# Performance work log

Measured on AMD Instinct MI355X. Metric: run time of the kernel, lower is better.

## Reference

```python
import jax, jax.numpy as jnp
import numpy as np
import math

D_MODEL = 1024
NUM_HEADS = 16
B, S = 2, 2048


def setup_inputs() -> dict:
    key = jax.random.key(0)
    ks = jax.random.split(key, 12)
    s = 0.02
    inp = {
        "q": jax.random.normal(ks[0], (B, S, D_MODEL), jnp.float32),
        "k": jax.random.normal(ks[1], (B, S, D_MODEL), jnp.float32),
        "v": jax.random.normal(ks[2], (B, S, D_MODEL), jnp.float32),
        "W_q": jax.random.normal(ks[3], (D_MODEL, D_MODEL), jnp.float32) * s,
        "b_q": jnp.zeros((D_MODEL,), jnp.float32),
        "W_k": jax.random.normal(ks[4], (D_MODEL, D_MODEL), jnp.float32) * s,
        "b_k": jnp.zeros((D_MODEL,), jnp.float32),
        "W_v": jax.random.normal(ks[5], (D_MODEL, D_MODEL), jnp.float32) * s,
        "b_v": jnp.zeros((D_MODEL,), jnp.float32),
        "W_o": jax.random.normal(ks[6], (D_MODEL, D_MODEL), jnp.float32) * s,
        "b_o": jnp.zeros((D_MODEL,), jnp.float32),
        # broadcastable causal mask [1,1,S,S]; masked positions are 0
        "mask": jnp.tril(jnp.ones((S, S), jnp.int32))[None, None, :, :],
    }
    return inp


def reference(q, k, v, W_q, b_q, W_k, b_k, W_v, b_v, W_o, b_o, mask):
    H, d_k = NUM_HEADS, D_MODEL // NUM_HEADS
    Bq, Sq, D = q.shape
    Sk = k.shape[1]
    # Linear projections (torch Linear: x @ W.T + b), split heads -> [B,H,S,d_k]
    qh = (q @ W_q.T + b_q).reshape(Bq, Sq, H, d_k).transpose(0, 2, 1, 3)
    kh = (k @ W_k.T + b_k).reshape(Bq, Sk, H, d_k).transpose(0, 2, 1, 3)
    vh = (v @ W_v.T + b_v).reshape(Bq, Sk, H, d_k).transpose(0, 2, 1, 3)
    # scores [B,H,Sq,Sk]
    scores = jnp.einsum("bhqd,bhkd->bhqk", qh, kh) / math.sqrt(d_k)
    scores = jnp.where(mask == 0, jnp.float32(-jnp.inf), scores)
    attn = jax.nn.softmax(scores, axis=-1)
    context = jnp.einsum("bhqk,bhkd->bhqd", attn, vh)
    context = context.transpose(0, 2, 1, 3).reshape(Bq, Sq, D)
    return context @ W_o.T + b_o
```

## Files before the change

kernel.cpp:

```cpp
#include <hip/hip_runtime.h>
#include <hip/hip_bf16.h>

using f32x4  = __attribute__((ext_vector_type(4))) float;
using short8 = __attribute__((ext_vector_type(8))) short;
using us8    = __attribute__((ext_vector_type(8))) unsigned short;
using us4    = __attribute__((ext_vector_type(4))) unsigned short;
using fl4    = __attribute__((ext_vector_type(4))) float;

__device__ __forceinline__ unsigned short f2bf(float f){
    unsigned u = __builtin_bit_cast(unsigned, f);
    u += 0x7FFF + ((u >> 16) & 1);
    return (unsigned short)(u >> 16);
}

__device__ __forceinline__ void gload16(const unsigned short* g, unsigned short* l) {
    __builtin_amdgcn_global_load_lds(
        (const __attribute__((address_space(1))) unsigned int*)g,
        (__attribute__((address_space(3))) unsigned int*)l, 16, 0, 0);
}

__global__ __launch_bounds__(256)
void conv_bf16(const float* __restrict__ s0, const float* __restrict__ s1, const float* __restrict__ s2,
               const float* __restrict__ s3, const float* __restrict__ s4, const float* __restrict__ s5,
               const float* __restrict__ s6,
               unsigned short* __restrict__ d0, unsigned short* __restrict__ d1, unsigned short* __restrict__ d2,
               unsigned short* __restrict__ d3, unsigned short* __restrict__ d4, unsigned short* __restrict__ d5,
               unsigned short* __restrict__ d6,
               int nbig4, int nsml4)
{
    const int z = blockIdx.z;
    const float* s = (z==0)?s0:(z==1)?s1:(z==2)?s2:(z==3)?s3:(z==4)?s4:(z==5)?s5:s6;
    unsigned short* d = (z==0)?d0:(z==1)?d1:(z==2)?d2:(z==3)?d3:(z==4)?d4:(z==5)?d5:d6;
    const int n4 = (z < 3) ? nbig4 : nsml4;
    const int stride = gridDim.x * blockDim.x;
    for (int i = blockIdx.x * blockDim.x + threadIdx.x; i < n4; i += stride) {
        fl4 v = ((const fl4*)s)[i];
        us4 o = { f2bf(v[0]), f2bf(v[1]), f2bf(v[2]), f2bf(v[3]) };
        ((us4*)d)[i] = o;
    }
}

template<bool OBF16>
__global__ __launch_bounds__(256, 2)
void gemm_bf16(const unsigned short* __restrict__ A0, const unsigned short* __restrict__ A1,
               const unsigned short* __restrict__ A2,
               const unsigned short* __restrict__ W0, const unsigned short* __restrict__ W1,
               const unsigned short* __restrict__ W2,
               const float* __restrict__ B0, const float* __restrict__ B1, const float* __restrict__ B2,
               void* __restrict__ O0, void* __restrict__ O1, void* __restrict__ O2,
               int M, int N, int K)
{
    const int z = blockIdx.z;
    const unsigned short* Ap = (z==0)?A0:(z==1)?A1:A2;
    const unsigned short* Wp = (z==0)?W0:(z==1)?W1:W2;
    const float* bp = (z==0)?B0:(z==1)?B1:B2;
    void* Op = (z==0)?O0:(z==1)?O1:O2;

    const int tid = threadIdx.x, lane = tid & 63, w = tid >> 6;
    const int wr = w >> 1, wc = w & 1;
    const int l15 = lane & 15, l4 = lane >> 4;
    const int bm = blockIdx.y, bn = blockIdx.x;

    __shared__ unsigned short As[2][128 * 64];
    __shared__ unsigned short Bs[2][128 * 64];

    f32x4 acc[4][4];
    #pragma unroll
    for (int i = 0; i < 4; i++)
        #pragma unroll
        for (int j = 0; j < 4; j++) acc[i][j] = (f32x4){0.f, 0.f, 0.f, 0.f};

    const int KT = K >> 6;
    const int srow = lane >> 3;
    const int scol = (lane & 7) * 8;

    auto stage = [&](int buf, int kt) {
        #pragma unroll
        for (int i = 0; i < 4; i++) {
            const int chunk = w * 4 + i;
            const int row = chunk * 8 + srow;
            gload16(Ap + (size_t)(bm * 128 + row) * K + kt * 64 + scol, &As[buf][chunk * 512]);
            gload16(Wp + (size_t)(bn * 128 + row) * K + kt * 64 + scol, &Bs[buf][chunk * 512]);
        }
    };

    stage(0, 0);
    int cur = 0;
    for (int kt = 0; kt < KT; ++kt) {
        if (kt + 1 < KT) {
            stage(cur ^ 1, kt + 1);
            asm volatile("s_waitcnt vmcnt(8)" ::: "memory");
        } else {
            asm volatile("s_waitcnt vmcnt(0)" ::: "memory");
        }
        __builtin_amdgcn_s_barrier();

        short8 af[4][2], bfr[4][2];
        #pragma unroll
        for (int mf = 0; mf < 4; mf++)
            #pragma unroll
            for (int kf = 0; kf < 2; kf++)
                af[mf][kf] = *(const short8*)&As[cur][(wr * 64 + mf * 16 + l15) * 64 + kf * 32 + l4 * 8];
        #pragma unroll
        for (int nf = 0; nf < 4; nf++)
            #pragma unroll
            for (int kf = 0; kf < 2; kf++)
                bfr[nf][kf] = *(const short8*)&Bs[cur][(wc * 64 + nf * 16 + l15) * 64 + kf * 32 + l4 * 8];
        #pragma unroll
        for (int mf = 0; mf < 4; mf++)
            #pragma unroll
            for (int nf = 0; nf < 4; nf++)
                #pragma unroll
                for (int kf = 0; kf < 2; kf++)
                    acc[mf][nf] = __builtin_amdgcn_mfma_f32_16x16x32_bf16(af[mf][kf], bfr[nf][kf], acc[mf][nf], 0, 0, 0);

        __builtin_amdgcn_s_barrier();
        cur ^= 1;
    }

    #pragma unroll
    for (int mf = 0; mf < 4; mf++) {
        int row = bm * 128 + wr * 64 + mf * 16 + l4 * 4;
        #pragma unroll
        for (int nf = 0; nf < 4; nf++) {
            int col = bn * 128 + wc * 64 + nf * 16 + l15;
            float bv = bp[col];
            #pragma unroll
            for (int r = 0; r < 4; r++) {
                float vv = acc[mf][nf][r] + bv;
                if constexpr (OBF16)
                    ((unsigned short*)Op)[(size_t)(row + r) * N + col] = f2bf(vv);
                else
                    ((float*)Op)[(size_t)(row + r) * N + col] = vv;
            }
        }
    }
}

__global__ __launch_bounds__(256, 2)
void attn_causal(const unsigned short* __restrict__ Qp,
                 const unsigned short* __restrict__ Kp,
                 const unsigned short* __restrict__ Vp,
                 unsigned short* __restrict__ Ctx)
{
    const int S = 2048, D = 1024;
    const int bh = blockIdx.y, b = bh >> 4, h = bh & 15;
    const int pairIdx = blockIdx.x;
    const int tid = threadIdx.x, w = tid >> 6, lane = tid & 63;
    const int l15 = lane & 15, l4 = lane >> 4;

    __shared__ unsigned short Ks[64 * 64];
    __shared__ unsigned short Vt[64 * 64];
    __shared__ unsigned short Ps[4][16 * 64];

    const float sc = 0.125f * 1.44269504088896f;

    for (int phase = 0; phase < 2; ++phase) {
        const int qt = (phase == 0) ? pairIdx : 31 - pairIdx;
        const int nt = qt + 1;
        const int qbase = qt * 64 + w * 16;
        const int qrow = qbase + l15;

        short8 qf[2];
        #pragma unroll
        for (int kf = 0; kf < 2; kf++)
            qf[kf] = *(const short8*)(Qp + (size_t)(b * S + qrow) * D + h * 64 + kf * 32 + l4 * 8);

        float mrow = -3.0e38f, lrow = 0.f;
        f32x4 oacc[4];
        #pragma unroll
        for (int df = 0; df < 4; df++) oacc[df] = (f32x4){0.f, 0.f, 0.f, 0.f};

        us8 krg[2], vrg[2];
        #pragma unroll
        for (int i = 0; i < 2; i++) {
            int cc = i * 256 + tid, r = cc >> 3, d0 = (cc & 7) * 8;
            krg[i] = *(const us8*)(Kp + (size_t)(b * S + r) * D + h * 64 + d0);
            vrg[i] = *(const us8*)(Vp + (size_t)(b * S + r) * D + h * 64 + d0);
        }

        for (int t = 0; t < nt; ++t) {
            __syncthreads();
            #pragma unroll
            for (int i = 0; i < 2; i++) {
                int cc = i * 256 + tid, r = cc >> 3, e = cc & 7, d0 = e * 8;
                int koff = (r * 128 + d0 * 2) ^ ((r & 7) << 4);
                *(us8*)((char*)Ks + koff) = krg[i];
                #pragma unroll
                for (int j = 0; j < 8; j++) {
                    int voff = ((d0 + j) * 128 + r * 2) ^ (e << 4);
                    *(unsigned short*)((char*)Vt + voff) = vrg[i][j];
                }
            }
            __syncthreads();

            if (t + 1 < nt) {
                #pragma unroll
                for (int i = 0; i < 2; i++) {
                    int cc = i * 256 + tid, r = cc >> 3, d0 = (cc & 7) * 8;
                    krg[i] = *(const us8*)(Kp + (size_t)(b * S + (t + 1) * 64 + r) * D + h * 64 + d0);
                    vrg[i] = *(const us8*)(Vp + (size_t)(b * S + (t + 1) * 64 + r) * D + h * 64 + d0);
                }
            }

            f32x4 sf[4];
            #pragma unroll
            for (int nf = 0; nf < 4; nf++) sf[nf] = (f32x4){0.f, 0.f, 0.f, 0.f};
            #pragma unroll
            for (int nf = 0; nf < 4; nf++)
                #pragma unroll
                for (int kf = 0; kf < 2; kf++) {
                    int row = nf * 16 + l15;
                    int off = (row * 128 + kf * 64 + l4 * 16) ^ ((row & 7) << 4);
                    short8 kfrag = *(const short8*)((const char*)Ks + off);
                    sf[nf] = __builtin_amdgcn_mfma_f32_16x16x32_bf16(kfrag, qf[kf], sf[nf], 0, 0, 0);
                }

            float pf[16];
            const bool domask = (t == nt - 1);
            #pragma unroll
            for (int nf = 0; nf < 4; nf++)
                #pragma unroll
                for (int r = 0; r < 4; r++) {
                    float x = sf[nf][r] * sc;
                    if (domask) {
                        int kv = t * 64 + nf * 16 + l4 * 4 + r;
                        if (kv > qrow) x = -3.0e38f;
                    }
                    pf[nf * 4 + r] = x;
                }

            float t8[8];
            #pragma unroll
            for (int i = 0; i < 8; i++) t8[i] = fmaxf(pf[i], pf[i + 8]);
            float t4a = fmaxf(t8[0], t8[4]), t4b = fmaxf(t8[1], t8[5]);
            float t4c = fmaxf(t8[2], t8[6]), t4d = fmaxf(t8[3], t8[7]);
            float pm = fmaxf(fmaxf(t4a, t4b), fmaxf(t4c, t4d));
            pm = fmaxf(pm, __shfl_xor(pm, 16));
            pm = fmaxf(pm, __shfl_xor(pm, 32));
            float mn = fmaxf(mrow, pm);
            float fs = exp2f(mrow - mn);
            float ps = 0.f;
            #pragma unroll
            for (int i = 0; i < 16; i++) { float e = exp2f(pf[i] - mn); pf[i] = e; ps += e; }
            ps += __shfl_xor(ps, 16);
            ps += __shfl_xor(ps, 32);
            lrow = lrow * fs + ps;
            mrow = mn;

            float fsq[4];
            #pragma unroll
            for (int r = 0; r < 4; r++) fsq[r] = __shfl(fs, l4 * 4 + r);
            #pragma unroll
            for (int df = 0; df < 4; df++)
                #pragma unroll
                for (int r = 0; r < 4; r++) oacc[df][r] *= fsq[r];

            #pragma unroll
            for (int nf = 0; nf < 4; nf++) {
                us4 pk = { f2bf(pf[nf * 4 + 0]), f2bf(pf[nf * 4 + 1]),
                           f2bf(pf[nf * 4 + 2]), f2bf(pf[nf * 4 + 3]) };
                int off = (l15 * 128 + (nf * 16 + l4 * 4) * 2) ^ ((l15 & 7) << 4);
                *(us4*)((char*)Ps[w] + off) = pk;
            }

            #pragma unroll
            for (int kf = 0; kf < 2; kf++) {
                int offp = (l15 * 128 + kf * 64 + l4 * 16) ^ ((l15 & 7) << 4);
                short8 pa = *(const short8*)((const char*)Ps[w] + offp);
                #pragma unroll
                for (int df = 0; df < 4; df++) {
                    int d = df * 16 + l15;
                    int offv = (d * 128 + kf * 64 + l4 * 16) ^ (((d >> 3) & 7) << 4);
                    short8 vb = *(const short8*)((const char*)Vt + offv);
                    oacc[df] = __builtin_amdgcn_mfma_f32_16x16x32_bf16(pa, vb, oacc[df], 0, 0, 0);
                }
            }
        }

        float inv = 1.0f / lrow;
        float invq[4];
        #pragma unroll
        for (int r = 0; r < 4; r++) invq[r] = __shfl(inv, l4 * 4 + r);
        #pragma unroll
        for (int df = 0; df < 4; df++)
            #pragma unroll
            for (int r = 0; r < 4; r++) {
                int row = qt * 64 + w * 16 + l4 * 4 + r;
                Ctx[(size_t)(b * S + row) * D + h * 64 + df * 16 + l15] = f2bf(oacc[df][r] * invq[r]);
            }
    }
}

extern "C" void kernel_launch(void* const* d_in, const int* in_sizes, int n_in,
                              void* d_out, int out_size, void* d_ws, size_t ws_size,
                              hipStream_t stream)
{
    const float* q  = (const float*)d_in[0];
    const float* k  = (const float*)d_in[1];
    const float* v  = (const float*)d_in[2];
    const float* Wq = (const float*)d_in[3];
    const float* bq = (const float*)d_in[4];
    const float* Wk = (const float*)d_in[5];
    const float* bk = (const float*)d_in[6];
    const float* Wv = (const float*)d_in[7];
    const float* bv = (const float*)d_in[8];
    const float* Wo = (const float*)d_in[9];
    const float* bo = (const float*)d_in[10];

    const int M = 4096, N = 1024, K = 1024;
    const size_t nBS = (size_t)M * N;
    const size_t nW  = (size_t)N * K;

    unsigned short* qb  = (unsigned short*)d_ws;
    unsigned short* kb  = qb  + nBS;
    unsigned short* vb  = kb  + nBS;
    unsigned short* Wqb = vb  + nBS;
    unsigned short* Wkb = Wqb + nW;
    unsigned short* Wvb = Wkb + nW;
    unsigned short* Wob = Wvb + nW;
    unsigned short* Qp  = Wob + nW;
    unsigned short* Kp  = Qp  + nBS;
    unsigned short* Vp  = Kp  + nBS;
    unsigned short* Ct  = qb;

    dim3 gc(1024, 1, 7);
    conv_bf16<<<gc, 256, 0, stream>>>(q, k, v, Wq, Wk, Wv, Wo,
                                      qb, kb, vb, Wqb, Wkb, Wvb, Wob,
                                      (int)(nBS / 4), (int)(nW / 4));

    dim3 g1(N / 128, M / 128, 3);
    gemm_bf16<true><<<g1, 256, 0, stream>>>(qb, kb, vb, Wqb, Wkb, Wvb,
                                            bq, bk, bv, Qp, Kp, Vp, M, N, K);

    dim3 g2(16, 32);
    attn_causal<<<g2, 256, 0, stream>>>(Qp, Kp, Vp, Ct);

    dim3 g3(N / 128, M / 128, 1);
    gemm_bf16<false><<<g3, 256, 0, stream>>>(Ct, Ct, Ct, Wob, Wob, Wob,
                                             bo, bo, bo, d_out, d_out, d_out, M, N, K);
}
```

Measured before the change: 263.8 us.

## Rework causal attention around 32x32 MFMA with pre-transposed V and register-resident P

Attention now uses 32x32x16 bf16 MFMA with two waves of 32 query rows each (128 threads), instead of 16x16 tiles across four waves. V is transposed once by a separate kernel so the tile load into LDS becomes vectorized rather than a scatter of single elements. The P matrix stays in registers, packed with v_cvt_pk_bf16_f32 and rearranged with v_permlane32_swap, which removes the LDS round trip for P. The cost is an extra kernel launch plus extra V traffic, and half as many threads per block, which lowers parallelism within each block.

```diff
diff --git a/kernel.cpp b/kernel.cpp
--- a/kernel.cpp
+++ b/kernel.cpp
@@ -2,6 +2,7 @@
 #include <hip/hip_bf16.h>
 
 using f32x4  = __attribute__((ext_vector_type(4))) float;
+using f32x16 = __attribute__((ext_vector_type(16))) float;
 using short8 = __attribute__((ext_vector_type(8))) short;
 using us8    = __attribute__((ext_vector_type(8))) unsigned short;
 using us4    = __attribute__((ext_vector_type(4))) unsigned short;
@@ -11,6 +12,16 @@
     unsigned u = __builtin_bit_cast(unsigned, f);
     u += 0x7FFF + ((u >> 16) & 1);
     return (unsigned short)(u >> 16);
+}
+
+__device__ __forceinline__ unsigned cvtpk_bf16(float lo, float hi){
+    unsigned r;
+    asm volatile("v_cvt_pk_bf16_f32 %0, %1, %2" : "=v"(r) : "v"(lo), "v"(hi));
+    return r;
+}
+
+__device__ __forceinline__ void pl32swap(unsigned &a, unsigned &b){
+    asm volatile("v_permlane32_swap_b32 %0, %1" : "+v"(a), "+v"(b));
 }
 
 __device__ __forceinline__ void gload16(const unsigned short* g, unsigned short* l) {
@@ -137,157 +148,191 @@
     }
 }
 
-__global__ __launch_bounds__(256, 2)
+__global__ __launch_bounds__(256)
+void transpose_v(const unsigned short* __restrict__ Vp, unsigned short* __restrict__ VpT)
+{
+    const int bh = blockIdx.y, b = bh >> 4, h = bh & 15;
+    const int s0 = blockIdx.x * 64;
+    const int tid = threadIdx.x;
+    __shared__ unsigned short T[64 * 64];
+    #pragma unroll
+    for (int i = 0; i < 2; i++) {
+        int cc = i * 256 + tid, r = cc >> 3, c = cc & 7;
+        us8 v = *(const us8*)(Vp + (size_t)(b * 2048 + s0 + r) * 1024 + h * 64 + c * 8);
+        int off = (r * 128 + c * 16) ^ ((((r & 7) ^ ((r >> 3) & 7))) << 4);
+        *(us8*)((char*)T + off) = v;
+    }
+    __syncthreads();
+    #pragma unroll
+    for (int i = 0; i < 2; i++) {
+        int cc = i * 256 + tid, d = cc >> 3, c = cc & 7;
+        us8 o;
+        #pragma unroll
+        for (int j = 0; j < 8; j++) {
+            int s = c * 8 + j;
+            int off = (s * 128 + d * 2) ^ ((((s & 7) ^ ((s >> 3) & 7))) << 4);
+            o[j] = *(const unsigned short*)((const char*)T + off);
+        }
+        *(us8*)(VpT + ((size_t)bh * 64 + d) * 2048 + s0 + c * 8) = o;
+    }
+}
+
+__global__ __launch_bounds__(128)
 void attn_causal(const unsigned short* __restrict__ Qp,
                  const unsigned short* __restrict__ Kp,
-                 const unsigned short* __restrict__ Vp,
+                 const unsigned short* __restrict__ VpT,
                  unsigned short* __restrict__ Ctx)
 {
     const int S = 2048, D = 1024;
     const int bh = blockIdx.y, b = bh >> 4, h = bh & 15;
     const int pairIdx = blockIdx.x;
     const int tid = threadIdx.x, w = tid >> 6, lane = tid & 63;
-    const int l15 = lane & 15, l4 = lane >> 4;
+    const int l31 = lane & 31, hi = lane >> 5;
 
     __shared__ unsigned short Ks[64 * 64];
     __shared__ unsigned short Vt[64 * 64];
-    __shared__ unsigned short Ps[4][16 * 64];
 
     const float sc = 0.125f * 1.44269504088896f;
 
     for (int phase = 0; phase < 2; ++phase) {
         const int qt = (phase == 0) ? pairIdx : 31 - pairIdx;
         const int nt = qt + 1;
-        const int qbase = qt * 64 + w * 16;
-        const int qrow = qbase + l15;
-
-        short8 qf[2];
-        #pragma unroll
-        for (int kf = 0; kf < 2; kf++)
-            qf[kf] = *(const short8*)(Qp + (size_t)(b * S + qrow) * D + h * 64 + kf * 32 + l4 * 8);
+        const int qrow = qt * 64 + w * 32 + l31;
+
+        short8 qf[4];
+        #pragma unroll
+        for (int ks = 0; ks < 4; ks++)
+            qf[ks] = *(const short8*)(Qp + (size_t)(b * S + qrow) * D + h * 64 + ks * 16 + hi * 8);
 
         float mrow = -3.0e38f, lrow = 0.f;
-        f32x4 oacc[4];
-        #pragma unroll
-        for (int df = 0; df < 4; df++) oacc[df] = (f32x4){0.f, 0.f, 0.f, 0.f};
-
-        us8 krg[2], vrg[2];
-        #pragma unroll
-        for (int i = 0; i < 2; i++) {
-            int cc = i * 256 + tid, r = cc >> 3, d0 = (cc & 7) * 8;
-            krg[i] = *(const us8*)(Kp + (size_t)(b * S + r) * D + h * 64 + d0);
-            vrg[i] = *(const us8*)(Vp + (size_t)(b * S + r) * D + h * 64 + d0);
+        f32x16 oacc[2];
+        #pragma unroll
+        for (int dh = 0; dh < 2; dh++)
+            #pragma unroll
+            for (int r = 0; r < 16; r++) oacc[dh][r] = 0.f;
+
+        us8 krg[4], vtrg[4];
+        #pragma unroll
+        for (int i = 0; i < 4; i++) {
+            int cc = i * 128 + tid, r = cc >> 3, c = cc & 7;
+            krg[i]  = *(const us8*)(Kp  + (size_t)(b * S + r) * D + h * 64 + c * 8);
+            vtrg[i] = *(const us8*)(VpT + ((size_t)bh * 64 + r) * 2048 + c * 8);
         }
 
         for (int t = 0; t < nt; ++t) {
             __syncthreads();
             #pragma unroll
-            for (int i = 0; i < 2; i++) {
-                int cc = i * 256 + tid, r = cc >> 3, e = cc & 7, d0 = e * 8;
-                int koff = (r * 128 + d0 * 2) ^ ((r & 7) << 4);
-                *(us8*)((char*)Ks + koff) = krg[i];
-                #pragma unroll
-                for (int j = 0; j < 8; j++) {
-                    int voff = ((d0 + j) * 128 + r * 2) ^ (e << 4);
-                    *(unsigned short*)((char*)Vt + voff) = vrg[i][j];
-                }
+            for (int i = 0; i < 4; i++) {
+                int cc = i * 128 + tid, r = cc >> 3, c = cc & 7;
+                int off = (r * 128 + c * 16) ^ ((r & 7) << 4);
+                *(us8*)((char*)Ks + off) = krg[i];
+                *(us8*)((char*)Vt + off) = vtrg[i];
             }
             __syncthreads();
 
             if (t + 1 < nt) {
                 #pragma unroll
-                for (int i = 0; i < 2; i++) {
-                    int cc = i * 256 + tid, r = cc >> 3, d0 = (cc & 7) * 8;
-                    krg[i] = *(const us8*)(Kp + (size_t)(b * S + (t + 1) * 64 + r) * D + h * 64 + d0);
-                    vrg[i] = *(const us8*)(Vp + (size_t)(b * S + (t + 1) * 64 + r) * D + h * 64 + d0);
-                }
-            }
-
-            f32x4 sf[4];
-            #pragma unroll
-            for (int nf = 0; nf < 4; nf++) sf[nf] = (f32x4){0.f, 0.f, 0.f, 0.f};
-            #pragma unroll
-            for (int nf = 0; nf < 4; nf++)
-                #pragma unroll
-                for (int kf = 0; kf < 2; kf++) {
-                    int row = nf * 16 + l15;
-                    int off = (row * 128 + kf * 64 + l4 * 16) ^ ((row & 7) << 4);
+                for (int i = 0; i < 4; i++) {
+                    int cc = i * 128 + tid, r = cc >> 3, c = cc & 7;
+                    krg[i]  = *(const us8*)(Kp  + (size_t)(b * S + (t + 1) * 64 + r) * D + h * 64 + c * 8);
+                    vtrg[i] = *(const us8*)(VpT + ((size_t)bh * 64 + r) * 2048 + (t + 1) * 64 + c * 8);
+                }
+            }
+
+            f32x16 sacc[2];
+            #pragma unroll
+            for (int kvh = 0; kvh < 2; kvh++)
+                #pragma unroll
+                for (int r = 0; r < 16; r++) sacc[kvh][r] = 0.f;
+            #pragma unroll
+            for (int kvh = 0; kvh < 2; kvh++)
+                #pragma unroll
+                for (int ks = 0; ks < 4; ks++) {
+                    int row = kvh * 32 + l31;
+                    int off = (row * 128 + ks * 32 + hi * 16) ^ ((l31 & 7) << 4);
                     short8 kfrag = *(const short8*)((const char*)Ks + off);
-                    sf[nf] = __builtin_amdgcn_mfma_f32_16x16x32_bf16(kfrag, qf[kf], sf[nf], 0, 0, 0);
-                }
-
-            float pf[16];
+                    sacc[kvh] = __builtin_amdgcn_mfma_f32_32x32x16_bf16(kfrag, qf[ks], sacc[kvh], 0, 0, 0);
+                }
+
+            float pf[2][16];
             const bool domask = (t == nt - 1);
             #pragma unroll
-            for (int nf = 0; nf < 4; nf++)
-                #pragma unroll
-                for (int r = 0; r < 4; r++) {
-                    float x = sf[nf][r] * sc;
+            for (int kvh = 0; kvh < 2; kvh++)
+                #pragma unroll
+                for (int r = 0; r < 16; r++) {
+                    float x = sacc[kvh][r] * sc;
                     if (domask) {
-                        int kv = t * 64 + nf * 16 + l4 * 4 + r;
+                        int kv = t * 64 + kvh * 32 + (r & 3) + 8 * (r >> 2) + 4 * hi;
                         if (kv > qrow) x = -3.0e38f;
                     }
-                    pf[nf * 4 + r] = x;
-                }
-
-            float t8[8];
-            #pragma unroll
-            for (int i = 0; i < 8; i++) t8[i] = fmaxf(pf[i], pf[i + 8]);
-            float t4a = fmaxf(t8[0], t8[4]), t4b = fmaxf(t8[1], t8[5]);
-            float t4c = fmaxf(t8[2], t8[6]), t4d = fmaxf(t8[3], t8[7]);
-            float pm = fmaxf(fmaxf(t4a, t4b), fmaxf(t4c, t4d));
-            pm = fmaxf(pm, __shfl_xor(pm, 16));
+                    pf[kvh][r] = x;
+                }
+
+            float pm = -3.0e38f;
+            #pragma unroll
+            for (int kvh = 0; kvh < 2; kvh++)
+                #pragma unroll
+                for (int r = 0; r < 16; r++) pm = fmaxf(pm, pf[kvh][r]);
             pm = fmaxf(pm, __shfl_xor(pm, 32));
             float mn = fmaxf(mrow, pm);
             float fs = exp2f(mrow - mn);
             float ps = 0.f;
             #pragma unroll
-            for (int i = 0; i < 16; i++) { float e = exp2f(pf[i] - mn); pf[i] = e; ps += e; }
-            ps += __shfl_xor(ps, 16);
+            for (int kvh = 0; kvh < 2; kvh++)
+                #pragma unroll
+                for (int r = 0; r < 16; r++) {
+                    float e = exp2f(pf[kvh][r] - mn);
+                    pf[kvh][r] = e;
+                    ps += e;
+                }
             ps += __shfl_xor(ps, 32);
             lrow = lrow * fs + ps;
             mrow = mn;
-
-            float fsq[4];
-            #pragma unroll
-            for (int r = 0; r < 4; r++) fsq[r] = __shfl(fs, l4 * 4 + r);
-            #pragma unroll
-            for (int df = 0; df < 4; df++)
-                #pragma unroll
-                for (int r = 0; r < 4; r++) oacc[df][r] *= fsq[r];
-
-            #pragma unroll
-            for (int nf = 0; nf < 4; nf++) {
-                us4 pk = { f2bf(pf[nf * 4 + 0]), f2bf(pf[nf * 4 + 1]),
-                           f2bf(pf[nf * 4 + 2]), f2bf(pf[nf * 4 + 3]) };
-                int off = (l15 * 128 + (nf * 16 + l4 * 4) * 2) ^ ((l15 & 7) << 4);
-                *(us4*)((char*)Ps[w] + off) = pk;
-            }
-
-            #pragma unroll
-            for (int kf = 0; kf < 2; kf++) {
-                int offp = (l15 * 128 + kf * 64 + l4 * 16) ^ ((l15 & 7) << 4);
-                short8 pa = *(const short8*)((const char*)Ps[w] + offp);
-                #pragma unroll
-                for (int df = 0; df < 4; df++) {
-                    int d = df * 16 + l15;
-                    int offv = (d * 128 + kf * 64 + l4 * 16) ^ (((d >> 3) & 7) << 4);
-                    short8 vb = *(const short8*)((const char*)Vt + offv);
-                    oacc[df] = __builtin_amdgcn_mfma_f32_16x16x32_bf16(pa, vb, oacc[df], 0, 0, 0);
-                }
-            }
-        }
-
-        float inv = 1.0f / lrow;
-        float invq[4];
-        #pragma unroll
-        for (int r = 0; r < 4; r++) invq[r] = __shfl(inv, l4 * 4 + r);
-        #pragma unroll
-        for (int df = 0; df < 4; df++)
-            #pragma unroll
-            for (int r = 0; r < 4; r++) {
-                int row = qt * 64 + w * 16 + l4 * 4 + r;
-                Ctx[(size_t)(b * S + row) * D + h * 64 + df * 16 + l15] = f2bf(oacc[df][r] * invq[r]);
+            #pragma unroll
+            for (int dh = 0; dh < 2; dh++)
+                #pragma unroll
+                for (int r = 0; r < 16; r++) oacc[dh][r] *= fs;
+
+            #pragma unroll
+            for (int kvh = 0; kvh < 2; kvh++) {
+                unsigned w00 = cvtpk_bf16(pf[kvh][0],  pf[kvh][1]);
+                unsigned w01 = cvtpk_bf16(pf[kvh][2],  pf[kvh][3]);
+                unsigned w10 = cvtpk_bf16(pf[kvh][4],  pf[kvh][5]);
+                unsigned w11 = cvtpk_bf16(pf[kvh][6],  pf[kvh][7]);
+                unsigned w20 = cvtpk_bf16(pf[kvh][8],  pf[kvh][9]);
+                unsigned w21 = cvtpk_bf16(pf[kvh][10], pf[kvh][11]);
+                unsigned w30 = cvtpk_bf16(pf[kvh][12], pf[kvh][13]);
+                unsigned w31 = cvtpk_bf16(pf[kvh][14], pf[kvh][15]);
+                pl32swap(w00, w10);
+                pl32swap(w01, w11);
+                pl32swap(w20, w30);
+                pl32swap(w21, w31);
+                unsigned stepA[4] = { w00, w01, w10, w11 };
+                unsigned stepB[4] = { w20, w21, w30, w31 };
+                short8 bA = __builtin_bit_cast(short8, *(const us8*)stepA);
+                short8 bB = __builtin_bit_cast(short8, *(const us8*)stepB);
+                #pragma unroll
+                for (int dh = 0; dh < 2; dh++) {
+                    int row = dh * 32 + l31;
+                    int offA = (row * 128 + kvh * 64 + hi * 16) ^ ((l31 & 7) << 4);
+                    short8 vA = *(const short8*)((const char*)Vt + offA);
+                    oacc[dh] = __builtin_amdgcn_mfma_f32_32x32x16_bf16(vA, bA, oacc[dh], 0, 0, 0);
+                    int offB = offA ^ 32;
+                    short8 vB = *(const short8*)((const char*)Vt + offB);
+                    oacc[dh] = __builtin_amdgcn_mfma_f32_32x32x16_bf16(vB, bB, oacc[dh], 0, 0, 0);
+                }
+            }
+        }
+
+        float invl = 1.0f / lrow;
+        #pragma unroll
+        for (int dh = 0; dh < 2; dh++)
+            #pragma unroll
+            for (int tq = 0; tq < 4; tq++) {
+                us4 o = { f2bf(oacc[dh][4*tq+0] * invl), f2bf(oacc[dh][4*tq+1] * invl),
+                          f2bf(oacc[dh][4*tq+2] * invl), f2bf(oacc[dh][4*tq+3] * invl) };
+                int d = dh * 32 + tq * 8 + hi * 4;
+                *(us4*)(Ctx + (size_t)(b * S + qrow) * D + h * 64 + d) = o;
             }
     }
 }
@@ -312,17 +357,18 @@
     const size_t nBS = (size_t)M * N;
     const size_t nW  = (size_t)N * K;
 
-    unsigned short* qb  = (unsigned short*)d_ws;
-    unsigned short* kb  = qb  + nBS;
-    unsigned short* vb  = kb  + nBS;
-    unsigned short* Wqb = vb  + nBS;
-    unsigned short* Wkb = Wqb + nW;
-    unsigned short* Wvb = Wkb + nW;
-    unsigned short* Wob = Wvb + nW;
-    unsigned short* Qp  = Wob + nW;
-    unsigned short* Kp  = Qp  + nBS;
-    unsigned short* Vp  = Kp  + nBS;
-    unsigned short* Ct  = qb;
+    unsigned short* qb   = (unsigned short*)d_ws;
+    unsigned short* kb   = qb  + nBS;
+    unsigned short* vb   = kb  + nBS;
+    unsigned short* Wqb  = vb  + nBS;
+    unsigned short* Wkb  = Wqb + nW;
+    unsigned short* Wvb  = Wkb + nW;
+    unsigned short* Wob  = Wvb + nW;
+    unsigned short* Qp   = Wob + nW;
+    unsigned short* Kp   = Qp  + nBS;
+    unsigned short* Vp   = Kp  + nBS;
+    unsigned short* VpT  = Vp  + nBS;
+    unsigned short* Ct   = qb;
 
     dim3 gc(1024, 1, 7);
     conv_bf16<<<gc, 256, 0, stream>>>(q, k, v, Wq, Wk, Wv, Wo,
@@ -333,8 +379,11 @@
     gemm_bf16<true><<<g1, 256, 0, stream>>>(qb, kb, vb, Wqb, Wkb, Wvb,
                                             bq, bk, bv, Qp, Kp, Vp, M, N, K);
 
+    dim3 gt(32, 32);
+    transpose_v<<<gt, 256, 0, stream>>>(Vp, VpT);
+
     dim3 g2(16, 32);
-    attn_causal<<<g2, 256, 0, stream>>>(Qp, Kp, Vp, Ct);
+    attn_causal<<<g2, 128, 0, stream>>>(Qp, Kp, VpT, Ct);
 
     dim3 g3(N / 128, M / 128, 1);
     gemm_bf16<false><<<g3, 256, 0, stream>>>(Ct, Ct, Ct, Wob, Wob, Wob,
```

Result: no change. 268.5 us (+1.8%).
